# Optimization experiments

Hardware: AMD Instinct MI355X
Metric: run time of the kernel (lower is better)

The kernel has to match this reference:

```python
import jax, jax.numpy as jnp
import numpy as np

T, D, I, E, G, LG, K = 2048, 1024, 512, 32, 8, 4, 6
SI = 2 * I  # shared expert inter dim = n_shared_experts * inter_dim
ROUTE_SCALE = 1.0


def setup_inputs() -> dict:
    key = jax.random.key(0)
    ks = jax.random.split(key, 16)
    s = 0.02
    f = jnp.float32
    return {
        "x": jax.random.normal(ks[0], (T, D), f),
        "router_w": jax.random.normal(ks[1], (E, D), f) * s,
        "router_b": jax.random.normal(ks[2], (E,), f) * s,
        "W1": jax.random.normal(ks[3], (E, D, I), f) * s,
        "b1": jax.random.normal(ks[4], (E, I), f) * s,
        "W2": jax.random.normal(ks[5], (E, D, I), f) * s,
        "b2": jax.random.normal(ks[6], (E, I), f) * s,
        "W3": jax.random.normal(ks[7], (E, I, D), f) * s,
        "b3": jax.random.normal(ks[8], (E, D), f) * s,
        "sw1": jax.random.normal(ks[9], (D, SI), f) * s,
        "sb1": jax.random.normal(ks[10], (SI,), f) * s,
        "sw2": jax.random.normal(ks[11], (D, SI), f) * s,
        "sb2": jax.random.normal(ks[12], (SI,), f) * s,
        "sw3": jax.random.normal(ks[13], (SI, D), f) * s,
        "sb3": jax.random.normal(ks[14], (D,), f) * s,
    }


def _route(x, router_w, router_b):
    # Router: softmax scores (fp32), group-limited top-k.
    logits = x @ router_w.T + router_b                      # [T, E]
    scores = jax.nn.softmax(logits.astype(jnp.float32), axis=-1)
    original = scores
    sg = scores.reshape(x.shape[0], G, E // G)              # [T, G, E/G]
    # no router bias -> group score = sum of top-2 expert scores per group
    group_scores = jnp.sum(jax.lax.top_k(sg, 2)[0], axis=-1)  # [T, G]
    _, gidx = jax.lax.top_k(group_scores, LG)               # [T, LG]
    keep = jnp.zeros((x.shape[0], G), bool).at[jnp.arange(x.shape[0])[:, None], gidx].set(True)
    masked = jnp.where(keep[:, :, None], sg, -jnp.inf).reshape(x.shape[0], E)
    _, idx = jax.lax.top_k(masked, K)                       # [T, K]
    vals = jnp.take_along_axis(original, idx, axis=1) * ROUTE_SCALE
    return vals.astype(x.dtype), idx


def reference(x, router_w, router_b, W1, b1, W2, b2, W3, b3, sw1, sb1, sw2, sb2, sw3, sb3):
    vals, idx = _route(x, router_w, router_b)
    # dense gate matrix [T, E]; top-k indices per row are distinct
    gates = jnp.zeros((x.shape[0], E), x.dtype).at[jnp.arange(x.shape[0])[:, None], idx].set(vals)
    # routed experts: Expert(x) = W3 @ silu(w1(x) * w2(x))
    h1 = jnp.einsum('td,edi->tei', x, W1) + b1              # [T, E, I]
    h2 = jnp.einsum('td,edi->tei', x, W2) + b2
    h = jax.nn.silu(h1 * h2)
    y = jnp.einsum('tei,eid->td', h * gates[:, :, None], W3) + gates @ b3
    # shared expert
    z = jax.nn.silu((x @ sw1 + sb1) * (x @ sw2 + sb2)) @ sw3 + sb3
    return y + z
```

## Files before the change

### kernel.cpp

```cpp
#include <hip/hip_runtime.h>
#include <hip/hip_bf16.h>
#include <math.h>

#define T_CONST 2048
#define D_CONST 1024
#define I_CONST 512
#define SI_CONST 1024
#define E_CONST 32
#define G_CONST 8
#define LG_CONST 4
#define KSEL 6
#define BK 32

typedef __attribute__((ext_vector_type(8))) short short8;
typedef __attribute__((ext_vector_type(4))) float floatx4;

__device__ inline unsigned pack_bf16(float a, float b) {
  __hip_bfloat162 h = __float22bfloat162_rn(float2{a, b});
  return *reinterpret_cast<unsigned*>(&h);
}

__device__ inline void gload16(const void* g, void* l) {
  __builtin_amdgcn_global_load_lds(
      (const __attribute__((address_space(1))) unsigned int*)g,
      (__attribute__((address_space(3))) unsigned int*)l, 16, 0, 0);
}

__global__ __launch_bounds__(256) void cvt_x(const float* __restrict__ in,
                                             __hip_bfloat16* __restrict__ out) {
  size_t i = ((size_t)blockIdx.x * 256 + threadIdx.x) * 4;
  float4 v = *(const float4*)&in[i];
  uint2 u{pack_bf16(v.x, v.y), pack_bf16(v.z, v.w)};
  *(uint2*)&out[i] = u;
}

__global__ __launch_bounds__(256) void cvt_rwt(const float* __restrict__ rw,
                                               float* __restrict__ rwt) {
  int i = blockIdx.x * 256 + threadIdx.x;
  int d = i >> 5, e = i & 31;
  rwt[d * 32 + e] = rw[e * D_CONST + d];
}

__global__ __launch_bounds__(256) void transpose_all(
    const float* __restrict__ W1, const float* __restrict__ W2,
    const float* __restrict__ W3, const float* __restrict__ sw1,
    const float* __restrict__ sw2, const float* __restrict__ sw3,
    __hip_bfloat16* __restrict__ W1t, __hip_bfloat16* __restrict__ W2t,
    __hip_bfloat16* __restrict__ W3t, __hip_bfloat16* __restrict__ sw1t,
    __hip_bfloat16* __restrict__ sw2t, __hip_bfloat16* __restrict__ sw3t) {
  __shared__ float tile[64][65];
  int b = blockIdx.x;
  const float* in;
  __hip_bfloat16* out;
  int K, N, k0, n0;
  if (b < 8192) {
    int local = b & 4095;
    int mat = local >> 7, rem = local & 127;
    K = 1024; N = 512;
    in = ((b < 4096) ? W1 : W2) + (size_t)mat * (1024 * 512);
    out = ((b < 4096) ? W1t : W2t) + (size_t)mat * (1024 * 512);
    n0 = (rem & 7) * 64; k0 = (rem >> 3) * 64;
  } else if (b < 12288) {
    int local = b - 8192;
    int mat = local >> 7, rem = local & 127;
    K = 512; N = 1024;
    in = W3 + (size_t)mat * (512 * 1024);
    out = W3t + (size_t)mat * (512 * 1024);
    n0 = (rem & 15) * 64; k0 = (rem >> 4) * 64;
  } else {
    int local = b - 12288;
    int which = local >> 8, rem = local & 255;
    K = 1024; N = 1024;
    in = which == 0 ? sw1 : which == 1 ? sw2 : sw3;
    out = which == 0 ? sw1t : which == 1 ? sw2t : sw3t;
    n0 = (rem & 15) * 64; k0 = (rem >> 4) * 64;
  }
  int tid = threadIdx.x;
  int tr = tid >> 4, tc4 = (tid & 15) * 4;
#pragma unroll
  for (int i = 0; i < 4; ++i) {
    float4 v = *(const float4*)&in[(size_t)(k0 + tr + 16 * i) * N + n0 + tc4];
    tile[tr + 16 * i][tc4 + 0] = v.x;
    tile[tr + 16 * i][tc4 + 1] = v.y;
    tile[tr + 16 * i][tc4 + 2] = v.z;
    tile[tr + 16 * i][tc4 + 3] = v.w;
  }
  __syncthreads();
#pragma unroll
  for (int i = 0; i < 4; ++i) {
    int n = tr + 16 * i;
    unsigned lo = pack_bf16(tile[tc4 + 0][n], tile[tc4 + 1][n]);
    unsigned hi = pack_bf16(tile[tc4 + 2][n], tile[tc4 + 3][n]);
    uint2 u{lo, hi};
    *(uint2*)&out[(size_t)(n0 + n) * K + k0 + tc4] = u;
  }
}

__global__ __launch_bounds__(256) void router2(
    const float* __restrict__ x, const float* __restrict__ rwt,
    const float* __restrict__ rb, int* __restrict__ counts,
    int* __restrict__ stok, float* __restrict__ gatel) {
  const int lane = threadIdx.x & 63;
  const int wv = threadIdx.x >> 6;
  const int t = blockIdx.x * 4 + wv;
  const int e = lane & 31, h = lane >> 5;
  const float* xp = x + (size_t)t * D_CONST;
  float s = 0.f;
#pragma unroll 8
  for (int d = h; d < D_CONST; d += 2) s = fmaf(xp[d], rwt[d * 32 + e], s);
  s += __shfl_xor(s, 32);
  s += rb[e];
  float mx = s;
#pragma unroll
  for (int m = 16; m >= 1; m >>= 1) mx = fmaxf(mx, __shfl_xor(mx, m));
  float p = expf(s - mx);
  float sum = p;
#pragma unroll
  for (int m = 16; m >= 1; m >>= 1) sum += __shfl_xor(sum, m);
  float sc = p / sum;
  float a = sc, bb = __shfl_xor(a, 1);
  float hi = fmaxf(a, bb), lo = fminf(a, bb);
  float oh = __shfl_xor(hi, 2), ol = __shfl_xor(lo, 2);
  float gs = fmaxf(fmaxf(hi + oh, hi + lo), oh + ol);
  const int g = e >> 2;
  unsigned keep = 0;
  float gv = gs;
#pragma unroll
  for (int r = 0; r < LG_CONST; ++r) {
    float v = gv;
    int gi = g;
#pragma unroll
    for (int m = 16; m >= 1; m >>= 1) {
      float ov = __shfl_xor(v, m);
      int og = __shfl_xor(gi, m);
      if (ov > v || (ov == v && og < gi)) { v = ov; gi = og; }
    }
    keep |= 1u << gi;
    if (g == gi) gv = -1e30f;
  }
  float cand = ((keep >> g) & 1u) ? sc : -1e30f;
  int sel_e = -1;
  float sel_v = 0.f;
#pragma unroll
  for (int r = 0; r < KSEL; ++r) {
    float v = cand;
    int ei = e;
#pragma unroll
    for (int m = 16; m >= 1; m >>= 1) {
      float ov = __shfl_xor(v, m);
      int oe = __shfl_xor(ei, m);
      if (ov > v || (ov == v && oe < ei)) { v = ov; ei = oe; }
    }
    if (lane == r) { sel_e = ei; sel_v = v; }
    if (e == ei) cand = -1e30f;
  }
  if (lane < KSEL) {
    int pos = atomicAdd(&counts[sel_e], 1);
    stok[sel_e * T_CONST + pos] = t;
    gatel[sel_e * T_CONST + pos] = sel_v;
  }
}

__global__ void scan_k(const int* __restrict__ counts, int* __restrict__ offsets) {
  if (threadIdx.x == 0) {
    int s = 0;
    for (int e = 0; e < E_CONST; ++e) { offsets[e] = s; s += counts[e]; }
    offsets[E_CONST] = s;
  }
}

__global__ __launch_bounds__(256) void gather_x(
    const __hip_bfloat16* __restrict__ xbf, const int* __restrict__ counts,
    const int* __restrict__ offsets, const int* __restrict__ stok,
    const float* __restrict__ gatel, __hip_bfloat16* __restrict__ Xg,
    int* __restrict__ ctok, float* __restrict__ cgate) {
  int e = blockIdx.x;
  int cnt = counts[e];
  int row = blockIdx.y * 16 + (threadIdx.x >> 4);
  if (row >= cnt) return;
  int seg = threadIdx.x & 15;
  int tok = stok[e * T_CONST + row];
  int dst = offsets[e] + row;
  const uint4* src = (const uint4*)(xbf + (size_t)tok * D_CONST);
  uint4* d = (uint4*)(Xg + (size_t)dst * D_CONST);
#pragma unroll
  for (int i = 0; i < 8; ++i) d[i * 16 + seg] = src[i * 16 + seg];
  if (seg == 0) { ctok[dst] = tok; cgate[dst] = gatel[e * T_CONST + row]; }
}

__global__ __launch_bounds__(256, 2) void up_fused(
    const __hip_bfloat16* __restrict__ Xg, const __hip_bfloat16* __restrict__ xbf,
    const __hip_bfloat16* __restrict__ W1t, const __hip_bfloat16* __restrict__ W2t,
    const __hip_bfloat16* __restrict__ sw1t, const __hip_bfloat16* __restrict__ sw2t,
    const float* __restrict__ b1, const float* __restrict__ b2,
    const float* __restrict__ sb1, const float* __restrict__ sb2,
    const int* __restrict__ counts, const int* __restrict__ offsets,
    __hip_bfloat16* __restrict__ He, __hip_bfloat16* __restrict__ Hs) {
  const int z = blockIdx.z;
  const bool SH = (z == E_CONST);
  const int N = SH ? SI_CONST : I_CONST;
  const int n0 = blockIdx.x * 128;
  if (n0 >= N) return;
  const int cnt = SH ? T_CONST : counts[z];
  const int m0 = blockIdx.y * 128;
  if (m0 >= cnt) return;
  const int base = SH ? 0 : offsets[z];

  const __hip_bfloat16* Ab = SH ? (xbf + (size_t)m0 * D_CONST)
                                : (Xg + (size_t)(base + m0) * D_CONST);
  const __hip_bfloat16* B1 = SH ? (sw1t + (size_t)n0 * D_CONST)
                                : (W1t + ((size_t)z * I_CONST + n0) * D_CONST);
  const __hip_bfloat16* B2 = SH ? (sw2t + (size_t)n0 * D_CONST)
                                : (W2t + ((size_t)z * I_CONST + n0) * D_CONST);

  __shared__ short As[3 * 4096], Bs1[3 * 4096], Bs2[3 * 4096];

  const int tid = threadIdx.x, lane = tid & 63, wv = tid >> 6;
  const int l15 = lane & 15, quad = lane >> 4;
  const int wm = wv & 1, wn = wv >> 1;
  const int lr = lane >> 2;
  const int lc = lane & 3;

  const __hip_bfloat16 *aG[2], *b1G[2], *b2G[2];
#pragma unroll
  for (int i = 0; i < 2; ++i) {
    int r = wv * 32 + i * 16 + lr;
    int kap = lc ^ ((r >> 1) & 3);
    aG[i]  = Ab + (size_t)r * D_CONST + kap * 8;
    b1G[i] = B1 + (size_t)r * D_CONST + kap * 8;
    b2G[i] = B2 + (size_t)r * D_CONST + kap * 8;
  }
  const int ldsu = wv * 1024 + lane * 8;

  floatx4 acc1[4][4] = {};
  floatx4 acc2[4][4] = {};

  const int nIter = D_CONST / BK;

  auto stage = [&](int slot, int kk) {
    const int sb = slot * 4096;
#pragma unroll
    for (int i = 0; i < 2; ++i) {
      gload16(aG[i] + kk,  &As [sb + ldsu + i * 512]);
      gload16(b1G[i] + kk, &Bs1[sb + ldsu + i * 512]);
      gload16(b2G[i] + kk, &Bs2[sb + ldsu + i * 512]);
    }
  };

  stage(0, 0);
  stage(1, BK);
  int sl0 = 0, sl1 = 1, sl2 = 2;

  for (int s = 0; s < nIter; ++s) {
    int kn = (s + 2 < nIter) ? (s + 2) * BK : (nIter - 1) * BK;
    stage(sl2, kn);
    asm volatile("s_waitcnt vmcnt(12)" ::: "memory");
    __builtin_amdgcn_s_barrier();
    const int sb = sl0 * 4096;
    short8 a[4], x1[4], x2[4];
#pragma unroll
    for (int mi = 0; mi < 4; ++mi) {
      int m = wm * 64 + mi * 16 + l15;
      a[mi] = *(const short8*)&As[sb + m * 32 + (quad ^ ((m >> 1) & 3)) * 8];
    }
#pragma unroll
    for (int ni = 0; ni < 4; ++ni) {
      int n = wn * 64 + ni * 16 + l15;
      int u = sb + n * 32 + (quad ^ ((n >> 1) & 3)) * 8;
      x1[ni] = *(const short8*)&Bs1[u];
      x2[ni] = *(const short8*)&Bs2[u];
    }
    __builtin_amdgcn_s_setprio(1);
#pragma unroll
    for (int mi = 0; mi < 4; ++mi)
#pragma unroll
      for (int ni = 0; ni < 4; ++ni) {
        acc1[mi][ni] = __builtin_amdgcn_mfma_f32_16x16x32_bf16(a[mi], x1[ni], acc1[mi][ni], 0, 0, 0);
        acc2[mi][ni] = __builtin_amdgcn_mfma_f32_16x16x32_bf16(a[mi], x2[ni], acc2[mi][ni], 0, 0, 0);
      }
    __builtin_amdgcn_s_setprio(0);
    __builtin_amdgcn_s_barrier();
    int t = sl0; sl0 = sl1; sl1 = sl2; sl2 = t;
  }
  asm volatile("s_waitcnt vmcnt(0)" ::: "memory");

  const float* pb1 = SH ? sb1 : (b1 + (size_t)z * I_CONST);
  const float* pb2 = SH ? sb2 : (b2 + (size_t)z * I_CONST);
  __hip_bfloat16* outp = SH ? (Hs + (size_t)m0 * SI_CONST + n0)
                            : (He + (size_t)(base + m0) * I_CONST + n0);
  const int ldo = SH ? SI_CONST : I_CONST;
  float c1[4], c2[4];
#pragma unroll
  for (int ni = 0; ni < 4; ++ni) {
    int n = wn * 64 + ni * 16 + l15;
    c1[ni] = pb1[n0 + n];
    c2[ni] = pb2[n0 + n];
  }
#pragma unroll
  for (int mi = 0; mi < 4; ++mi) {
#pragma unroll
    for (int reg = 0; reg < 4; ++reg) {
      int m = wm * 64 + mi * 16 + quad * 4 + reg;
      if (m0 + m >= cnt) continue;
#pragma unroll
      for (int ni = 0; ni < 4; ++ni) {
        int n = wn * 64 + ni * 16 + l15;
        float h1 = acc1[mi][ni][reg] + c1[ni];
        float h2 = acc2[mi][ni][reg] + c2[ni];
        float p = h1 * h2;
        float s = p / (1.f + expf(-p));
        outp[(size_t)m * ldo + n] = __float2bfloat16(s);
      }
    }
  }
}

__global__ __launch_bounds__(256, 3) void down_fused(
    const __hip_bfloat16* __restrict__ He, const __hip_bfloat16* __restrict__ Hs,
    const __hip_bfloat16* __restrict__ W3t, const __hip_bfloat16* __restrict__ sw3t,
    const float* __restrict__ b3, const float* __restrict__ sb3,
    const int* __restrict__ counts, const int* __restrict__ offsets,
    const int* __restrict__ ctok, const float* __restrict__ cgate,
    float* __restrict__ out) {
  const int z = blockIdx.z;
  const bool SH = (z == E_CONST);
  const int n0 = blockIdx.x * 128;
  const int cnt = SH ? T_CONST : counts[z];
  const int m0 = blockIdx.y * 128;
  if (m0 >= cnt) return;
  const int base = SH ? 0 : offsets[z];
  const int Kd = SH ? SI_CONST : I_CONST;

  const __hip_bfloat16* Ab = SH ? (Hs + (size_t)m0 * SI_CONST)
                                : (He + (size_t)(base + m0) * I_CONST);
  const __hip_bfloat16* Bb = SH ? (sw3t + (size_t)n0 * SI_CONST)
                                : (W3t + ((size_t)z * D_CONST + n0) * I_CONST);

  __shared__ short As[3 * 4096], Bs[3 * 4096];

  const int tid = threadIdx.x, lane = tid & 63, wv = tid >> 6;
  const int l15 = lane & 15, quad = lane >> 4;
  const int wm = wv & 1, wn = wv >> 1;
  const int lr = lane >> 2, lc = lane & 3;

  const __hip_bfloat16 *aG[2], *bG[2];
#pragma unroll
  for (int i = 0; i < 2; ++i) {
    int r = wv * 32 + i * 16 + lr;
    int kap = lc ^ ((r >> 1) & 3);
    aG[i] = Ab + (size_t)r * Kd + kap * 8;
    bG[i] = Bb + (size_t)r * Kd + kap * 8;
  }
  const int ldsu = wv * 1024 + lane * 8;

  floatx4 acc[4][4] = {};
  const int nIter = Kd / BK;

  auto stage = [&](int slot, int kk) {
    const int sb = slot * 4096;
#pragma unroll
    for (int i = 0; i < 2; ++i) {
      gload16(aG[i] + kk, &As[sb + ldsu + i * 512]);
      gload16(bG[i] + kk, &Bs[sb + ldsu + i * 512]);
    }
  };

  stage(0, 0);
  stage(1, BK);
  int sl0 = 0, sl1 = 1, sl2 = 2;

  for (int s = 0; s < nIter; ++s) {
    int kn = (s + 2 < nIter) ? (s + 2) * BK : (nIter - 1) * BK;
    stage(sl2, kn);
    asm volatile("s_waitcnt vmcnt(8)" ::: "memory");
    __builtin_amdgcn_s_barrier();
    const int sb = sl0 * 4096;
    short8 a[4], bbf[4];
#pragma unroll
    for (int mi = 0; mi < 4; ++mi) {
      int m = wm * 64 + mi * 16 + l15;
      a[mi] = *(const short8*)&As[sb + m * 32 + (quad ^ ((m >> 1) & 3)) * 8];
    }
#pragma unroll
    for (int ni = 0; ni < 4; ++ni) {
      int n = wn * 64 + ni * 16 + l15;
      bbf[ni] = *(const short8*)&Bs[sb + n * 32 + (quad ^ ((n >> 1) & 3)) * 8];
    }
    __builtin_amdgcn_s_setprio(1);
#pragma unroll
    for (int mi = 0; mi < 4; ++mi)
#pragma unroll
      for (int ni = 0; ni < 4; ++ni)
        acc[mi][ni] = __builtin_amdgcn_mfma_f32_16x16x32_bf16(a[mi], bbf[ni], acc[mi][ni], 0, 0, 0);
    __builtin_amdgcn_s_setprio(0);
    __builtin_amdgcn_s_barrier();
    int t = sl0; sl0 = sl1; sl1 = sl2; sl2 = t;
  }
  asm volatile("s_waitcnt vmcnt(0)" ::: "memory");

  float bias[4];
#pragma unroll
  for (int ni = 0; ni < 4; ++ni) {
    int n = n0 + wn * 64 + ni * 16 + l15;
    bias[ni] = SH ? sb3[n] : b3[(size_t)z * D_CONST + n];
  }
#pragma unroll
  for (int mi = 0; mi < 4; ++mi) {
#pragma unroll
    for (int reg = 0; reg < 4; ++reg) {
      int m = wm * 64 + mi * 16 + quad * 4 + reg;
      if (m0 + m >= cnt) continue;
      int tok;
      float gate;
      if (SH) { tok = m0 + m; gate = 1.f; }
      else { int grow = base + m0 + m; tok = ctok[grow]; gate = cgate[grow]; }
#pragma unroll
      for (int ni = 0; ni < 4; ++ni) {
        int n = n0 + wn * 64 + ni * 16 + l15;
        float v = gate * (acc[mi][ni][reg] + bias[ni]);
        atomicAdd(&out[(size_t)tok * D_CONST + n], v);
      }
    }
  }
}

extern "C" void kernel_launch(void* const* d_in, const int* in_sizes, int n_in,
                              void* d_out, int out_size, void* d_ws, size_t ws_size,
                              hipStream_t stream) {
  const float* x   = (const float*)d_in[0];
  const float* rw  = (const float*)d_in[1];
  const float* rb  = (const float*)d_in[2];
  const float* W1  = (const float*)d_in[3];
  const float* b1  = (const float*)d_in[4];
  const float* W2  = (const float*)d_in[5];
  const float* b2  = (const float*)d_in[6];
  const float* W3  = (const float*)d_in[7];
  const float* b3  = (const float*)d_in[8];
  const float* sw1 = (const float*)d_in[9];
  const float* sb1 = (const float*)d_in[10];
  const float* sw2 = (const float*)d_in[11];
  const float* sb2 = (const float*)d_in[12];
  const float* sw3 = (const float*)d_in[13];
  const float* sb3 = (const float*)d_in[14];
  float* out = (float*)d_out;

  char* w = (char*)d_ws;
  size_t off = 0;
  auto alloc = [&](size_t bytes) {
    char* p = w + off;
    off += (bytes + 255) & ~(size_t)255;
    return p;
  };
  int* counts = (int*)alloc(E_CONST * 4);
  int* offsets = (int*)alloc((E_CONST + 1) * 4);
  int* stok = (int*)alloc((size_t)E_CONST * T_CONST * 4);
  float* gatel = (float*)alloc((size_t)E_CONST * T_CONST * 4);
  float* rwt = (float*)alloc((size_t)D_CONST * E_CONST * 4);
  int* ctok = (int*)alloc((size_t)T_CONST * KSEL * 4);
  float* cgate = (float*)alloc((size_t)T_CONST * KSEL * 4);
  __hip_bfloat16* x_bf = (__hip_bfloat16*)alloc((size_t)T_CONST * D_CONST * 2);
  __hip_bfloat16* Xg = (__hip_bfloat16*)alloc((size_t)(T_CONST * KSEL + 128) * D_CONST * 2);
  __hip_bfloat16* W1t = (__hip_bfloat16*)alloc((size_t)E_CONST * D_CONST * I_CONST * 2);
  __hip_bfloat16* W2t = (__hip_bfloat16*)alloc((size_t)E_CONST * D_CONST * I_CONST * 2);
  __hip_bfloat16* W3t = (__hip_bfloat16*)alloc((size_t)E_CONST * I_CONST * D_CONST * 2);
  __hip_bfloat16* sw1t = (__hip_bfloat16*)alloc((size_t)D_CONST * SI_CONST * 2);
  __hip_bfloat16* sw2t = (__hip_bfloat16*)alloc((size_t)D_CONST * SI_CONST * 2);
  __hip_bfloat16* sw3t = (__hip_bfloat16*)alloc((size_t)SI_CONST * D_CONST * 2);
  __hip_bfloat16* He = (__hip_bfloat16*)alloc((size_t)(T_CONST * KSEL + 128) * I_CONST * 2);
  __hip_bfloat16* Hs = (__hip_bfloat16*)alloc((size_t)T_CONST * SI_CONST * 2);

  hipMemsetAsync(counts, 0, E_CONST * sizeof(int), stream);
  hipMemsetAsync(out, 0, (size_t)out_size * sizeof(float), stream);
  cvt_rwt<<<(D_CONST * E_CONST) / 256, 256, 0, stream>>>(rw, rwt);
  cvt_x<<<(T_CONST * D_CONST) / 1024, 256, 0, stream>>>(x, x_bf);
  transpose_all<<<13056, 256, 0, stream>>>(W1, W2, W3, sw1, sw2, sw3,
                                           W1t, W2t, W3t, sw1t, sw2t, sw3t);
  router2<<<T_CONST / 4, 256, 0, stream>>>(x, rwt, rb, counts, stok, gatel);
  scan_k<<<1, 64, 0, stream>>>(counts, offsets);
  gather_x<<<dim3(E_CONST, T_CONST / 16), 256, 0, stream>>>(
      x_bf, counts, offsets, stok, gatel, Xg, ctok, cgate);
  up_fused<<<dim3(8, 16, E_CONST + 1), 256, 0, stream>>>(
      Xg, x_bf, W1t, W2t, sw1t, sw2t, b1, b2, sb1, sb2, counts, offsets, He, Hs);
  down_fused<<<dim3(8, 16, E_CONST + 1), 256, 0, stream>>>(
      He, Hs, W3t, sw3t, b3, sb3, counts, offsets, ctok, cgate, out);
}
```

Baseline: 526.3 us.

## Compact MoE tile schedule, double-buffer GEMMs, replace atomics with combine pass

Adds a plan_build kernel that scans expert counts and emits a compact list of (expert, m-block, n-block) tiles, so the up and down GEMMs launch 1D grids with no empty blocks. The shared-expert tiles come first in each list. Both GEMMs drop from triple to double LDS buffering with higher occupancy targets. The down GEMM no longer does atomicAdd scatters into the output. The shared expert writes out directly, routed results go to a per-slot buffer (aliased over W1t), and a new combine kernel sums the K slots per token. This removes atomic contention and the output memset, at the cost of an extra pass over an fp32 [T*K, D] buffer, a shallower prefetch pipeline, and reliance on W1t being dead after the up GEMM.

```diff
diff --git a/kernel.cpp b/kernel.cpp
--- a/kernel.cpp
+++ b/kernel.cpp
@@ -161,11 +161,46 @@
   }
 }
 
-__global__ void scan_k(const int* __restrict__ counts, int* __restrict__ offsets) {
-  if (threadIdx.x == 0) {
-    int s = 0;
-    for (int e = 0; e < E_CONST; ++e) { offsets[e] = s; s += counts[e]; }
-    offsets[E_CONST] = s;
+__global__ __launch_bounds__(64) void plan_build(
+    const int* __restrict__ counts, int* __restrict__ offsets,
+    int* __restrict__ plan_up, int* __restrict__ plan_dn, int* __restrict__ meta) {
+  const int lane = threadIdx.x;
+  for (int i = lane; i < 128; i += 64) {
+    int ent = (E_CONST << 8) | i;
+    plan_up[i] = ent;
+    plan_dn[i] = ent;
+  }
+  int cnt = (lane < E_CONST) ? counts[lane] : 0;
+  int incl = cnt;
+#pragma unroll
+  for (int d = 1; d < 64; d <<= 1) {
+    int v = __shfl_up(incl, d);
+    if (lane >= d) incl += v;
+  }
+  if (lane < E_CONST) offsets[lane] = incl - cnt;
+  if (lane == E_CONST - 1) offsets[E_CONST] = incl;
+  int mbs = (cnt + 127) >> 7;
+  int pm = mbs;
+#pragma unroll
+  for (int d = 1; d < 64; d <<= 1) {
+    int v = __shfl_up(pm, d);
+    if (lane >= d) pm += v;
+  }
+  int pmex = pm - mbs;
+  if (lane < E_CONST) {
+    int ub = 128 + pmex * 4, db = 128 + pmex * 8;
+    for (int mb = 0; mb < mbs; ++mb) {
+#pragma unroll
+      for (int nb = 0; nb < 4; ++nb)
+        plan_up[ub + mb * 4 + nb] = (lane << 8) | (mb << 3) | nb;
+#pragma unroll
+      for (int nb = 0; nb < 8; ++nb)
+        plan_dn[db + mb * 8 + nb] = (lane << 8) | (mb << 3) | nb;
+    }
+  }
+  if (lane == E_CONST - 1) {
+    meta[0] = 128 + pm * 4;
+    meta[1] = 128 + pm * 8;
   }
 }
 
@@ -173,7 +208,7 @@
     const __hip_bfloat16* __restrict__ xbf, const int* __restrict__ counts,
     const int* __restrict__ offsets, const int* __restrict__ stok,
     const float* __restrict__ gatel, __hip_bfloat16* __restrict__ Xg,
-    int* __restrict__ ctok, float* __restrict__ cgate) {
+    float* __restrict__ cgate, int* __restrict__ tcnt, int* __restrict__ tslot) {
   int e = blockIdx.x;
   int cnt = counts[e];
   int row = blockIdx.y * 16 + (threadIdx.x >> 4);
@@ -185,25 +220,29 @@
   uint4* d = (uint4*)(Xg + (size_t)dst * D_CONST);
 #pragma unroll
   for (int i = 0; i < 8; ++i) d[i * 16 + seg] = src[i * 16 + seg];
-  if (seg == 0) { ctok[dst] = tok; cgate[dst] = gatel[e * T_CONST + row]; }
-}
-
-__global__ __launch_bounds__(256, 2) void up_fused(
+  if (seg == 0) {
+    cgate[dst] = gatel[e * T_CONST + row];
+    int sl = atomicAdd(&tcnt[tok], 1);
+    tslot[tok * 8 + sl] = dst;
+  }
+}
+
+__global__ __launch_bounds__(256, 3) void up_fused(
     const __hip_bfloat16* __restrict__ Xg, const __hip_bfloat16* __restrict__ xbf,
     const __hip_bfloat16* __restrict__ W1t, const __hip_bfloat16* __restrict__ W2t,
     const __hip_bfloat16* __restrict__ sw1t, const __hip_bfloat16* __restrict__ sw2t,
     const float* __restrict__ b1, const float* __restrict__ b2,
     const float* __restrict__ sb1, const float* __restrict__ sb2,
     const int* __restrict__ counts, const int* __restrict__ offsets,
+    const int* __restrict__ plan, const int* __restrict__ meta,
     __hip_bfloat16* __restrict__ He, __hip_bfloat16* __restrict__ Hs) {
-  const int z = blockIdx.z;
+  if ((int)blockIdx.x >= meta[0]) return;
+  const int ent = plan[blockIdx.x];
+  const int z = ent >> 8;
+  const int m0 = ((ent >> 3) & 31) * 128;
+  const int n0 = (ent & 7) * 128;
   const bool SH = (z == E_CONST);
-  const int N = SH ? SI_CONST : I_CONST;
-  const int n0 = blockIdx.x * 128;
-  if (n0 >= N) return;
   const int cnt = SH ? T_CONST : counts[z];
-  const int m0 = blockIdx.y * 128;
-  if (m0 >= cnt) return;
   const int base = SH ? 0 : offsets[z];
 
   const __hip_bfloat16* Ab = SH ? (xbf + (size_t)m0 * D_CONST)
@@ -213,7 +252,7 @@
   const __hip_bfloat16* B2 = SH ? (sw2t + (size_t)n0 * D_CONST)
                                 : (W2t + ((size_t)z * I_CONST + n0) * D_CONST);
 
-  __shared__ short As[3 * 4096], Bs1[3 * 4096], Bs2[3 * 4096];
+  __shared__ short As[2 * 4096], Bs1[2 * 4096], Bs2[2 * 4096];
 
   const int tid = threadIdx.x, lane = tid & 63, wv = tid >> 6;
   const int l15 = lane & 15, quad = lane >> 4;
@@ -248,15 +287,14 @@
   };
 
   stage(0, 0);
-  stage(1, BK);
-  int sl0 = 0, sl1 = 1, sl2 = 2;
+  int cur = 0;
 
   for (int s = 0; s < nIter; ++s) {
-    int kn = (s + 2 < nIter) ? (s + 2) * BK : (nIter - 1) * BK;
-    stage(sl2, kn);
-    asm volatile("s_waitcnt vmcnt(12)" ::: "memory");
+    int kn = (s + 1 < nIter) ? (s + 1) * BK : s * BK;
+    stage(cur ^ 1, kn);
+    asm volatile("s_waitcnt vmcnt(6)" ::: "memory");
     __builtin_amdgcn_s_barrier();
-    const int sb = sl0 * 4096;
+    const int sb = cur * 4096;
     short8 a[4], x1[4], x2[4];
 #pragma unroll
     for (int mi = 0; mi < 4; ++mi) {
@@ -280,7 +318,7 @@
       }
     __builtin_amdgcn_s_setprio(0);
     __builtin_amdgcn_s_barrier();
-    int t = sl0; sl0 = sl1; sl1 = sl2; sl2 = t;
+    cur ^= 1;
   }
   asm volatile("s_waitcnt vmcnt(0)" ::: "memory");
 
@@ -315,19 +353,20 @@
   }
 }
 
-__global__ __launch_bounds__(256, 3) void down_fused(
+__global__ __launch_bounds__(256, 4) void down_fused(
     const __hip_bfloat16* __restrict__ He, const __hip_bfloat16* __restrict__ Hs,
     const __hip_bfloat16* __restrict__ W3t, const __hip_bfloat16* __restrict__ sw3t,
     const float* __restrict__ b3, const float* __restrict__ sb3,
     const int* __restrict__ counts, const int* __restrict__ offsets,
-    const int* __restrict__ ctok, const float* __restrict__ cgate,
-    float* __restrict__ out) {
-  const int z = blockIdx.z;
+    const float* __restrict__ cgate, const int* __restrict__ plan,
+    const int* __restrict__ meta, float* __restrict__ Yp, float* __restrict__ out) {
+  if ((int)blockIdx.x >= meta[1]) return;
+  const int ent = plan[blockIdx.x];
+  const int z = ent >> 8;
+  const int m0 = ((ent >> 3) & 31) * 128;
+  const int n0 = (ent & 7) * 128;
   const bool SH = (z == E_CONST);
-  const int n0 = blockIdx.x * 128;
   const int cnt = SH ? T_CONST : counts[z];
-  const int m0 = blockIdx.y * 128;
-  if (m0 >= cnt) return;
   const int base = SH ? 0 : offsets[z];
   const int Kd = SH ? SI_CONST : I_CONST;
 
@@ -336,7 +375,7 @@
   const __hip_bfloat16* Bb = SH ? (sw3t + (size_t)n0 * SI_CONST)
                                 : (W3t + ((size_t)z * D_CONST + n0) * I_CONST);
 
-  __shared__ short As[3 * 4096], Bs[3 * 4096];
+  __shared__ short As[2 * 4096], Bs[2 * 4096];
 
   const int tid = threadIdx.x, lane = tid & 63, wv = tid >> 6;
   const int l15 = lane & 15, quad = lane >> 4;
@@ -366,15 +405,14 @@
   };
 
   stage(0, 0);
-  stage(1, BK);
-  int sl0 = 0, sl1 = 1, sl2 = 2;
+  int cur = 0;
 
   for (int s = 0; s < nIter; ++s) {
-    int kn = (s + 2 < nIter) ? (s + 2) * BK : (nIter - 1) * BK;
-    stage(sl2, kn);
-    asm volatile("s_waitcnt vmcnt(8)" ::: "memory");
+    int kn = (s + 1 < nIter) ? (s + 1) * BK : s * BK;
+    stage(cur ^ 1, kn);
+    asm volatile("s_waitcnt vmcnt(4)" ::: "memory");
     __builtin_amdgcn_s_barrier();
-    const int sb = sl0 * 4096;
+    const int sb = cur * 4096;
     short8 a[4], bbf[4];
 #pragma unroll
     for (int mi = 0; mi < 4; ++mi) {
@@ -394,7 +432,7 @@
         acc[mi][ni] = __builtin_amdgcn_mfma_f32_16x16x32_bf16(a[mi], bbf[ni], acc[mi][ni], 0, 0, 0);
     __builtin_amdgcn_s_setprio(0);
     __builtin_amdgcn_s_barrier();
-    int t = sl0; sl0 = sl1; sl1 = sl2; sl2 = t;
+    cur ^= 1;
   }
   asm volatile("s_waitcnt vmcnt(0)" ::: "memory");
 
@@ -410,18 +448,34 @@
     for (int reg = 0; reg < 4; ++reg) {
       int m = wm * 64 + mi * 16 + quad * 4 + reg;
       if (m0 + m >= cnt) continue;
-      int tok;
-      float gate;
-      if (SH) { tok = m0 + m; gate = 1.f; }
-      else { int grow = base + m0 + m; tok = ctok[grow]; gate = cgate[grow]; }
 #pragma unroll
       for (int ni = 0; ni < 4; ++ni) {
         int n = n0 + wn * 64 + ni * 16 + l15;
-        float v = gate * (acc[mi][ni][reg] + bias[ni]);
-        atomicAdd(&out[(size_t)tok * D_CONST + n], v);
+        float v = acc[mi][ni][reg] + bias[ni];
+        if (SH) {
+          out[(size_t)(m0 + m) * D_CONST + n] = v;
+        } else {
+          int grow = base + m0 + m;
+          Yp[(size_t)grow * D_CONST + n] = cgate[grow] * v;
+        }
       }
     }
   }
+}
+
+__global__ __launch_bounds__(256) void combine(
+    const float* __restrict__ Yp, const int* __restrict__ tslot,
+    float* __restrict__ out) {
+  const int t = blockIdx.x;
+  const int d = threadIdx.x * 4;
+  const int* ts = &tslot[t * 8];
+  float4 o = *(const float4*)&out[(size_t)t * D_CONST + d];
+#pragma unroll
+  for (int k = 0; k < KSEL; ++k) {
+    float4 y = *(const float4*)&Yp[(size_t)ts[k] * D_CONST + d];
+    o.x += y.x; o.y += y.y; o.z += y.z; o.w += y.w;
+  }
+  *(float4*)&out[(size_t)t * D_CONST + d] = o;
 }
 
 extern "C" void kernel_launch(void* const* d_in, const int* in_sizes, int n_in,
@@ -453,10 +507,14 @@
   };
   int* counts = (int*)alloc(E_CONST * 4);
   int* offsets = (int*)alloc((E_CONST + 1) * 4);
+  int* meta = (int*)alloc(16);
+  int* plan_up = (int*)alloc(768 * 4);
+  int* plan_dn = (int*)alloc(1280 * 4);
+  int* tcnt = (int*)alloc((size_t)T_CONST * 4);
+  int* tslot = (int*)alloc((size_t)T_CONST * 8 * 4);
   int* stok = (int*)alloc((size_t)E_CONST * T_CONST * 4);
   float* gatel = (float*)alloc((size_t)E_CONST * T_CONST * 4);
   float* rwt = (float*)alloc((size_t)D_CONST * E_CONST * 4);
-  int* ctok = (int*)alloc((size_t)T_CONST * KSEL * 4);
   float* cgate = (float*)alloc((size_t)T_CONST * KSEL * 4);
   __hip_bfloat16* x_bf = (__hip_bfloat16*)alloc((size_t)T_CONST * D_CONST * 2);
   __hip_bfloat16* Xg = (__hip_bfloat16*)alloc((size_t)(T_CONST * KSEL + 128) * D_CONST * 2);
@@ -468,19 +526,22 @@
   __hip_bfloat16* sw3t = (__hip_bfloat16*)alloc((size_t)SI_CONST * D_CONST * 2);
   __hip_bfloat16* He = (__hip_bfloat16*)alloc((size_t)(T_CONST * KSEL + 128) * I_CONST * 2);
   __hip_bfloat16* Hs = (__hip_bfloat16*)alloc((size_t)T_CONST * SI_CONST * 2);
+  float* Yp = (float*)W1t;
 
   hipMemsetAsync(counts, 0, E_CONST * sizeof(int), stream);
-  hipMemsetAsync(out, 0, (size_t)out_size * sizeof(float), stream);
+  hipMemsetAsync(tcnt, 0, (size_t)T_CONST * sizeof(int), stream);
   cvt_rwt<<<(D_CONST * E_CONST) / 256, 256, 0, stream>>>(rw, rwt);
   cvt_x<<<(T_CONST * D_CONST) / 1024, 256, 0, stream>>>(x, x_bf);
   transpose_all<<<13056, 256, 0, stream>>>(W1, W2, W3, sw1, sw2, sw3,
                                            W1t, W2t, W3t, sw1t, sw2t, sw3t);
   router2<<<T_CONST / 4, 256, 0, stream>>>(x, rwt, rb, counts, stok, gatel);
-  scan_k<<<1, 64, 0, stream>>>(counts, offsets);
+  plan_build<<<1, 64, 0, stream>>>(counts, offsets, plan_up, plan_dn, meta);
   gather_x<<<dim3(E_CONST, T_CONST / 16), 256, 0, stream>>>(
-      x_bf, counts, offsets, stok, gatel, Xg, ctok, cgate);
-  up_fused<<<dim3(8, 16, E_CONST + 1), 256, 0, stream>>>(
-      Xg, x_bf, W1t, W2t, sw1t, sw2t, b1, b2, sb1, sb2, counts, offsets, He, Hs);
-  down_fused<<<dim3(8, 16, E_CONST + 1), 256, 0, stream>>>(
-      He, Hs, W3t, sw3t, b3, sb3, counts, offsets, ctok, cgate, out);
-}
+      x_bf, counts, offsets, stok, gatel, Xg, cgate, tcnt, tslot);
+  up_fused<<<768, 256, 0, stream>>>(
+      Xg, x_bf, W1t, W2t, sw1t, sw2t, b1, b2, sb1, sb2, counts, offsets,
+      plan_up, meta, He, Hs);
+  down_fused<<<1280, 256, 0, stream>>>(
+      He, Hs, W3t, sw3t, b3, sb3, counts, offsets, cgate, plan_dn, meta, Yp, out);
+  combine<<<T_CONST, 256, 0, stream>>>(Yp, tslot, out);
+}
```

Result: slower. 603.4 us (+14.6%).
